# Kernel optimization log

Measured on AMD Instinct MI355X. Metric: run time of the kernel, lower is better.

## Reference

```python
import jax, jax.numpy as jnp
import numpy as np

N = 50000      # nodes
E = 800000     # edges
D_IN = 128     # embedding_dim
H = 4          # g_num_heads
D = 64         # g_hidden_dim (per head)
SLOPE = 0.2    # g_negative_slope


def setup_inputs() -> dict:
    key = jax.random.key(0)
    ks = jax.random.split(key, 16)
    def lin(k, fin, fout):
        return jax.random.normal(k, (fin, fout), jnp.float32) / np.float32(np.sqrt(fin))
    def att(k, heads):
        return jax.random.normal(k, (heads, D), jnp.float32) * np.float32(0.1)
    return {
        'x':  jax.random.normal(ks[0], (N, D_IN), jnp.float32),
        'src': jax.random.randint(ks[1], (E,), 0, N),
        'dst': jax.random.randint(ks[2], (E,), 0, N),
        'W0': lin(ks[3], D_IN, H * D), 'al0': att(ks[4], H), 'ar0': att(ks[5], H), 'b0': jnp.zeros((H * D,), jnp.float32),
        'W1': lin(ks[6], H * D, H * D), 'al1': att(ks[7], H), 'ar1': att(ks[8], H), 'b1': jnp.zeros((H * D,), jnp.float32),
        'W2': lin(ks[9], H * D, 1 * D), 'al2': att(ks[10], 1), 'ar2': att(ks[11], 1), 'b2': jnp.zeros((D,), jnp.float32),
    }


def gat_layer(x, W, al, ar, b, src, dst, heads, act):
    # x: [N, F_in] -> h: [N, heads, D]
    h = (x @ W).reshape(N, heads, D)
    el = jnp.sum(h * al, axis=-1)                      # [N, heads]
    er = jnp.sum(h * ar, axis=-1)                      # [N, heads]
    e = jax.nn.leaky_relu(el[src] + er[dst], SLOPE)    # [E, heads]
    # edge softmax over incoming edges of each dst node (numerically stable)
    m = jax.ops.segment_max(e, dst, num_segments=N)    # [N, heads]
    ee = jnp.exp(e - m[dst])
    z = jax.ops.segment_sum(ee, dst, num_segments=N)   # [N, heads]
    alpha = ee / z[dst]                                # [E, heads]
    # weighted aggregation of source features
    out = jax.ops.segment_sum(alpha[:, :, None] * h[src], dst, num_segments=N)  # [N, heads, D]
    out = out + b.reshape(1, heads, D)
    return jax.nn.elu(out) if act else out


def reference(x, src, dst, W0, al0, ar0, b0, W1, al1, ar1, b1, W2, al2, ar2, b2):
    f = gat_layer(x, W0, al0, ar0, b0, src, dst, H, True).reshape(N, H * D)
    f = gat_layer(f, W1, al1, ar1, b1, src, dst, H, True).reshape(N, H * D)
    out = gat_layer(f, W2, al2, ar2, b2, src, dst, 1, False).mean(axis=1)  # [N, D]
    return out
```

## Files before the change

kernel.cpp:

```cpp
#include <hip/hip_runtime.h>
#include <math.h>

#define NNODES 50000
#define NEDGES 800000


__global__ void k_zero_int(int* __restrict__ p, int n) {
  int i = blockIdx.x * blockDim.x + threadIdx.x;
  if (i < n) p[i] = 0;
}

__global__ void k_hist(const int* __restrict__ dst, int* __restrict__ deg) {
  int i = blockIdx.x * blockDim.x + threadIdx.x;
  if (i < NEDGES) atomicAdd(&deg[dst[i]], 1);
}

__global__ __launch_bounds__(1024) void k_scan(const int* __restrict__ deg,
                                               int* __restrict__ ptr,
                                               int* __restrict__ cur) {
  __shared__ int s_w[16];
  __shared__ int s_carry;
  const int tid = threadIdx.x;
  const int lane = tid & 63;
  const int wid = tid >> 6;
  if (tid == 0) s_carry = 0;
  __syncthreads();
  for (int base = 0; base < NNODES; base += 1024) {
    const int i = base + tid;
    const int v = (i < NNODES) ? deg[i] : 0;
    int x = v;
#pragma unroll
    for (int off = 1; off < 64; off <<= 1) {
      int t = __shfl_up(x, off);
      if (lane >= off) x += t;
    }
    if (lane == 63) s_w[wid] = x;
    __syncthreads();
    const int carry = s_carry;
    if (wid == 0) {
      int ws = (lane < 16) ? s_w[lane] : 0;
#pragma unroll
      for (int off = 1; off < 16; off <<= 1) {
        int t = __shfl_up(ws, off);
        if (lane >= off) ws += t;
      }
      if (lane < 16) s_w[lane] = ws;
    }
    __syncthreads();
    const int woff = (wid > 0) ? s_w[wid - 1] : 0;
    const int excl = carry + woff + (x - v);
    if (i < NNODES) {
      ptr[i] = excl;
      cur[i] = excl;
    }
    __syncthreads();
    if (tid == 0) s_carry = carry + s_w[15];
  }
  __syncthreads();
  if (tid == 0) ptr[NNODES] = s_carry;
}

__global__ void k_scatter(const int* __restrict__ src, const int* __restrict__ dst,
                          int* __restrict__ cur, int* __restrict__ csr) {
  int i = blockIdx.x * blockDim.x + threadIdx.x;
  if (i < NEDGES) {
    int d = dst[i];
    int p = atomicAdd(&cur[d], 1);
    csr[p] = src[i];
  }
}


template <int K, int NC, int BN>
__global__ __launch_bounds__(256) void k_gemm(const float* __restrict__ A,
                                              const float* __restrict__ B,
                                              float* __restrict__ C) {
  constexpr int BM = 128;
  constexpr int BK = 16;
  constexpr int TN = BN / 16;
  __shared__ float Ast[BK][BM + 4];
  __shared__ float Bs[BK][BN];
  const int tid = threadIdx.x;
  const int tx = tid & 15;
  const int ty = tid >> 4;
  const int rowBase = blockIdx.x * BM;
  const int colBase = blockIdx.y * BN;
  const int arow = tid >> 2;
  const int ak = (tid & 3) << 2;

  float acc[8][TN] = {};

  for (int k0 = 0; k0 < K; k0 += BK) {
#pragma unroll
    for (int rr = 0; rr < 2; ++rr) {
      const int r = arow + rr * 64;
      const int gr = rowBase + r;
      float4 av = make_float4(0.f, 0.f, 0.f, 0.f);
      if (gr < NNODES) av = *(const float4*)&A[(size_t)gr * K + k0 + ak];
      Ast[ak + 0][r] = av.x;
      Ast[ak + 1][r] = av.y;
      Ast[ak + 2][r] = av.z;
      Ast[ak + 3][r] = av.w;
    }
    if constexpr (BN == 128) {
      const int brow = tid >> 5;
      const int bcol = (tid & 31) << 2;
#pragma unroll
      for (int rr = 0; rr < 2; ++rr)
        *(float4*)&Bs[brow + rr * 8][bcol] =
            *(const float4*)&B[(size_t)(k0 + brow + rr * 8) * NC + colBase + bcol];
    } else {
      const int brow = tid >> 4;
      const int bcol = (tid & 15) << 2;
      *(float4*)&Bs[brow][bcol] =
          *(const float4*)&B[(size_t)(k0 + brow) * NC + colBase + bcol];
    }
    __syncthreads();
#pragma unroll
    for (int k = 0; k < BK; ++k) {
      float4 a0 = *(const float4*)&Ast[k][ty * 8];
      float4 a1 = *(const float4*)&Ast[k][ty * 8 + 4];
      float a[8] = {a0.x, a0.y, a0.z, a0.w, a1.x, a1.y, a1.z, a1.w};
      float b[TN];
      float4 b0 = *(const float4*)&Bs[k][tx * 4];
      b[0] = b0.x; b[1] = b0.y; b[2] = b0.z; b[3] = b0.w;
      if constexpr (TN == 8) {
        float4 b1 = *(const float4*)&Bs[k][64 + tx * 4];
        b[4] = b1.x; b[5] = b1.y; b[6] = b1.z; b[7] = b1.w;
      }
#pragma unroll
      for (int i = 0; i < 8; ++i)
#pragma unroll
        for (int j = 0; j < TN; ++j) acc[i][j] = fmaf(a[i], b[j], acc[i][j]);
    }
    __syncthreads();
  }
#pragma unroll
  for (int i = 0; i < 8; ++i) {
    const int r = rowBase + ty * 8 + i;
    if (r < NNODES) {
      {
        float4 o = make_float4(acc[i][0], acc[i][1], acc[i][2], acc[i][3]);
        *(float4*)&C[(size_t)r * NC + colBase + tx * 4] = o;
      }
      if constexpr (TN == 8) {
        float4 o = make_float4(acc[i][4], acc[i][5], acc[i][6], acc[i][7]);
        *(float4*)&C[(size_t)r * NC + colBase + 64 + tx * 4] = o;
      }
    }
  }
}


template <int HEADS>
__global__ __launch_bounds__(HEADS * 64) void k_elr(const float* __restrict__ h,
                                                    const float* __restrict__ al,
                                                    const float* __restrict__ ar,
                                                    float* __restrict__ el,
                                                    float* __restrict__ er) {
  const int n = blockIdx.x;
  const int tid = threadIdx.x;
  float hv = h[(size_t)n * HEADS * 64 + tid];
  float pl = hv * al[tid];
  float pr = hv * ar[tid];
#pragma unroll
  for (int m = 1; m < 64; m <<= 1) {
    pl += __shfl_xor(pl, m);
    pr += __shfl_xor(pr, m);
  }
  if ((tid & 63) == 0) {
    el[n * HEADS + (tid >> 6)] = pl;
    er[n * HEADS + (tid >> 6)] = pr;
  }
}


template <int HEADS, bool ACT>
__global__ __launch_bounds__(64) void k_aggregate(const float* __restrict__ h,
                                                  const float* __restrict__ el,
                                                  const float* __restrict__ er,
                                                  const int* __restrict__ ptr,
                                                  const int* __restrict__ csr,
                                                  const float* __restrict__ bias,
                                                  float* __restrict__ out) {
  constexpr int HD = HEADS * 64;
  constexpr int VEC = HEADS;
  constexpr int CH = 64 / HEADS;
  const int n = blockIdx.x;
  const int tid = threadIdx.x;
  const int head = tid / (64 / HEADS);
  const int beg = ptr[n];
  const int deg = ptr[n + 1] - beg;

  __shared__ float s_m[HEADS];
  __shared__ float s_z[HEADS];
  __shared__ int s_src[CH];
  __shared__ float s_w[64];

  {
    const int hh = tid & (HEADS - 1);
    const float ern = er[n * HEADS + hh];
    float mloc = -INFINITY;
    for (int i = tid / HEADS; i < deg; i += 64 / HEADS) {
      int s = csr[beg + i];
      float e = el[s * HEADS + hh] + ern;
      e = e > 0.f ? e : 0.2f * e;
      mloc = fmaxf(mloc, e);
    }
#pragma unroll
    for (int m = HEADS; m < 64; m <<= 1) mloc = fmaxf(mloc, __shfl_xor(mloc, m));
    float zloc = 0.f;
    for (int i = tid / HEADS; i < deg; i += 64 / HEADS) {
      int s = csr[beg + i];
      float e = el[s * HEADS + hh] + ern;
      e = e > 0.f ? e : 0.2f * e;
      zloc += expf(e - mloc);
    }
#pragma unroll
    for (int m = HEADS; m < 64; m <<= 1) zloc += __shfl_xor(zloc, m);
    if (tid < HEADS) { s_m[tid] = mloc; s_z[tid] = zloc; }
  }
  __syncthreads();
  const float invz = (deg > 0) ? 1.0f / s_z[head] : 0.f;

  float acc[VEC];
#pragma unroll
  for (int v = 0; v < VEC; ++v) acc[v] = 0.f;

  for (int c0 = 0; c0 < deg; c0 += CH) {
    const int cnt = min(CH, deg - c0);
    __syncthreads();
    {
      const int c = tid / HEADS;
      const int hh = tid & (HEADS - 1);
      if (c < cnt) {
        int s = csr[beg + c0 + c];
        if (hh == 0) s_src[c] = s;
        float e = el[s * HEADS + hh] + er[n * HEADS + hh];
        e = e > 0.f ? e : 0.2f * e;
        s_w[tid] = expf(e - s_m[hh]);
      }
    }
    __syncthreads();
    for (int c = 0; c < cnt; ++c) {
      const float w = s_w[c * HEADS + head];
      const float* hp = &h[(size_t)s_src[c] * HD + tid * VEC];
      if constexpr (VEC == 4) {
        float4 hv = *(const float4*)hp;
        acc[0] = fmaf(w, hv.x, acc[0]);
        acc[1] = fmaf(w, hv.y, acc[1]);
        acc[2] = fmaf(w, hv.z, acc[2]);
        acc[3] = fmaf(w, hv.w, acc[3]);
      } else {
        acc[0] = fmaf(w, hp[0], acc[0]);
      }
    }
  }

#pragma unroll
  for (int v = 0; v < VEC; ++v) {
    float r = acc[v] * invz + bias[tid * VEC + v];
    if (ACT) r = r > 0.f ? r : expm1f(r);
    acc[v] = r;
  }
  if constexpr (VEC == 4) {
    float4 o = make_float4(acc[0], acc[1], acc[2], acc[3]);
    *(float4*)&out[(size_t)n * HD + (tid << 2)] = o;
  } else {
    out[(size_t)n * HD + tid] = acc[0];
  }
}


extern "C" void kernel_launch(void* const* d_in, const int* in_sizes, int n_in,
                              void* d_out, int out_size, void* d_ws, size_t ws_size,
                              hipStream_t stream) {
  const float* x   = (const float*)d_in[0];
  const int*   src = (const int*)d_in[1];
  const int*   dst = (const int*)d_in[2];
  const float* W0  = (const float*)d_in[3];
  const float* al0 = (const float*)d_in[4];
  const float* ar0 = (const float*)d_in[5];
  const float* b0  = (const float*)d_in[6];
  const float* W1  = (const float*)d_in[7];
  const float* al1 = (const float*)d_in[8];
  const float* ar1 = (const float*)d_in[9];
  const float* b1  = (const float*)d_in[10];
  const float* W2  = (const float*)d_in[11];
  const float* al2 = (const float*)d_in[12];
  const float* ar2 = (const float*)d_in[13];
  const float* b2  = (const float*)d_in[14];
  float* out = (float*)d_out;

  float* hA = (float*)d_ws;
  float* fB = hA + (size_t)NNODES * 256;
  float* el = fB + (size_t)NNODES * 256;
  float* er = el + (size_t)NNODES * 4;
  int* deg  = (int*)(er + (size_t)NNODES * 4);
  int* ptr  = deg + NNODES;
  int* cur  = ptr + NNODES + 1;
  int* csr  = cur + NNODES;

  k_zero_int<<<(NNODES + 255) / 256, 256, 0, stream>>>(deg, NNODES);
  k_hist<<<(NEDGES + 255) / 256, 256, 0, stream>>>(dst, deg);
  k_scan<<<1, 1024, 0, stream>>>(deg, ptr, cur);
  k_scatter<<<(NEDGES + 255) / 256, 256, 0, stream>>>(src, dst, cur, csr);

  dim3 g128((NNODES + 127) / 128, 256 / 128);
  k_gemm<128, 256, 128><<<g128, 256, 0, stream>>>(x, W0, hA);
  k_elr<4><<<NNODES, 256, 0, stream>>>(hA, al0, ar0, el, er);
  k_aggregate<4, true><<<NNODES, 64, 0, stream>>>(hA, el, er, ptr, csr, b0, fB);
  k_gemm<256, 256, 128><<<g128, 256, 0, stream>>>(fB, W1, hA);
  k_elr<4><<<NNODES, 256, 0, stream>>>(hA, al1, ar1, el, er);
  k_aggregate<4, true><<<NNODES, 64, 0, stream>>>(hA, el, er, ptr, csr, b1, fB);
  dim3 g2((NNODES + 127) / 128, 1);
  k_gemm<256, 64, 64><<<g2, 256, 0, stream>>>(fB, W2, hA);
  k_elr<1><<<NNODES, 64, 0, stream>>>(hA, al2, ar2, el, er);
  k_aggregate<1, false><<<NNODES, 64, 0, stream>>>(hA, el, er, ptr, csr, b2, out);
}
```

Measured before the change: 753.2 us.

## Fuse attention logits into GEMM epilogue and single-pass edge softmax

Computes el/er dot products inside the GEMM epilogue with shuffle reductions, removing the separate k_elr kernels and their re-read of h. Adds register prefetch of the next A/B tile in the GEMM loop. Aggregation now computes exp(e) without subtracting the segment max and accumulates the softmax denominator alongside the weighted sum, eliminating two passes over each node's edges. This trades numerical-overflow safety for fewer passes.

```diff
diff --git a/kernel.cpp b/kernel.cpp
--- a/kernel.cpp
+++ b/kernel.cpp
@@ -71,10 +71,14 @@
 }
 
 
-template <int K, int NC, int BN>
+template <int K, int NC, int BN, int HEADS>
 __global__ __launch_bounds__(256) void k_gemm(const float* __restrict__ A,
                                               const float* __restrict__ B,
-                                              float* __restrict__ C) {
+                                              float* __restrict__ C,
+                                              const float* __restrict__ al,
+                                              const float* __restrict__ ar,
+                                              float* __restrict__ el,
+                                              float* __restrict__ er) {
   constexpr int BM = 128;
   constexpr int BK = 16;
   constexpr int TN = BN / 16;
@@ -87,40 +91,59 @@
   const int colBase = blockIdx.y * BN;
   const int arow = tid >> 2;
   const int ak = (tid & 3) << 2;
-
-  float acc[8][TN] = {};
-
-  for (int k0 = 0; k0 < K; k0 += BK) {
-#pragma unroll
-    for (int rr = 0; rr < 2; ++rr) {
-      const int r = arow + rr * 64;
-      const int gr = rowBase + r;
-      float4 av = make_float4(0.f, 0.f, 0.f, 0.f);
-      if (gr < NNODES) av = *(const float4*)&A[(size_t)gr * K + k0 + ak];
-      Ast[ak + 0][r] = av.x;
-      Ast[ak + 1][r] = av.y;
-      Ast[ak + 2][r] = av.z;
-      Ast[ak + 3][r] = av.w;
-    }
+  const bool v0 = (rowBase + arow) < NNODES;
+  const bool v1 = (rowBase + arow + 64) < NNODES;
+  const float* a0p = A + (size_t)(rowBase + arow) * K + ak;
+  const float* a1p = A + (size_t)(rowBase + arow + 64) * K + ak;
+
+  float4 avr[2];
+  float4 bvr[2];
+  const float4 z4 = make_float4(0.f, 0.f, 0.f, 0.f);
+
+  auto load_tile = [&](int k0) {
+    avr[0] = v0 ? *(const float4*)(a0p + k0) : z4;
+    avr[1] = v1 ? *(const float4*)(a1p + k0) : z4;
     if constexpr (BN == 128) {
       const int brow = tid >> 5;
       const int bcol = (tid & 31) << 2;
-#pragma unroll
-      for (int rr = 0; rr < 2; ++rr)
-        *(float4*)&Bs[brow + rr * 8][bcol] =
-            *(const float4*)&B[(size_t)(k0 + brow + rr * 8) * NC + colBase + bcol];
+      bvr[0] = *(const float4*)&B[(size_t)(k0 + brow) * NC + colBase + bcol];
+      bvr[1] = *(const float4*)&B[(size_t)(k0 + brow + 8) * NC + colBase + bcol];
     } else {
       const int brow = tid >> 4;
       const int bcol = (tid & 15) << 2;
-      *(float4*)&Bs[brow][bcol] =
-          *(const float4*)&B[(size_t)(k0 + brow) * NC + colBase + bcol];
-    }
-    __syncthreads();
+      bvr[0] = *(const float4*)&B[(size_t)(k0 + brow) * NC + colBase + bcol];
+    }
+  };
+
+  float acc[8][TN] = {};
+  load_tile(0);
+
+  for (int k0 = 0; k0 < K; k0 += BK) {
+#pragma unroll
+    for (int rr = 0; rr < 2; ++rr) {
+      const int r = arow + rr * 64;
+      Ast[ak + 0][r] = avr[rr].x;
+      Ast[ak + 1][r] = avr[rr].y;
+      Ast[ak + 2][r] = avr[rr].z;
+      Ast[ak + 3][r] = avr[rr].w;
+    }
+    if constexpr (BN == 128) {
+      const int brow = tid >> 5;
+      const int bcol = (tid & 31) << 2;
+      *(float4*)&Bs[brow][bcol] = bvr[0];
+      *(float4*)&Bs[brow + 8][bcol] = bvr[1];
+    } else {
+      const int brow = tid >> 4;
+      const int bcol = (tid & 15) << 2;
+      *(float4*)&Bs[brow][bcol] = bvr[0];
+    }
+    __syncthreads();
+    if (k0 + BK < K) load_tile(k0 + BK);
 #pragma unroll
     for (int k = 0; k < BK; ++k) {
-      float4 a0 = *(const float4*)&Ast[k][ty * 8];
-      float4 a1 = *(const float4*)&Ast[k][ty * 8 + 4];
-      float a[8] = {a0.x, a0.y, a0.z, a0.w, a1.x, a1.y, a1.z, a1.w};
+      float4 fa0 = *(const float4*)&Ast[k][ty * 8];
+      float4 fa1 = *(const float4*)&Ast[k][ty * 8 + 4];
+      float a[8] = {fa0.x, fa0.y, fa0.z, fa0.w, fa1.x, fa1.y, fa1.z, fa1.w};
       float b[TN];
       float4 b0 = *(const float4*)&Bs[k][tx * 4];
       b[0] = b0.x; b[1] = b0.y; b[2] = b0.z; b[3] = b0.w;
@@ -135,42 +158,52 @@
     }
     __syncthreads();
   }
+
+  const int head0 = colBase >> 6;
+  float4 alA = *(const float4*)&al[colBase + tx * 4];
+  float4 arA = *(const float4*)&ar[colBase + tx * 4];
+  float4 alB = z4, arB = z4;
+  if constexpr (TN == 8) {
+    alB = *(const float4*)&al[colBase + 64 + tx * 4];
+    arB = *(const float4*)&ar[colBase + 64 + tx * 4];
+  }
+
 #pragma unroll
   for (int i = 0; i < 8; ++i) {
     const int r = rowBase + ty * 8 + i;
-    if (r < NNODES) {
-      {
-        float4 o = make_float4(acc[i][0], acc[i][1], acc[i][2], acc[i][3]);
-        *(float4*)&C[(size_t)r * NC + colBase + tx * 4] = o;
-      }
+    const bool vr = r < NNODES;
+    if (vr) {
+      float4 o = make_float4(acc[i][0], acc[i][1], acc[i][2], acc[i][3]);
+      *(float4*)&C[(size_t)r * NC + colBase + tx * 4] = o;
       if constexpr (TN == 8) {
-        float4 o = make_float4(acc[i][4], acc[i][5], acc[i][6], acc[i][7]);
-        *(float4*)&C[(size_t)r * NC + colBase + 64 + tx * 4] = o;
-      }
-    }
-  }
-}
-
-
-template <int HEADS>
-__global__ __launch_bounds__(HEADS * 64) void k_elr(const float* __restrict__ h,
-                                                    const float* __restrict__ al,
-                                                    const float* __restrict__ ar,
-                                                    float* __restrict__ el,
-                                                    float* __restrict__ er) {
-  const int n = blockIdx.x;
-  const int tid = threadIdx.x;
-  float hv = h[(size_t)n * HEADS * 64 + tid];
-  float pl = hv * al[tid];
-  float pr = hv * ar[tid];
-#pragma unroll
-  for (int m = 1; m < 64; m <<= 1) {
-    pl += __shfl_xor(pl, m);
-    pr += __shfl_xor(pr, m);
-  }
-  if ((tid & 63) == 0) {
-    el[n * HEADS + (tid >> 6)] = pl;
-    er[n * HEADS + (tid >> 6)] = pr;
+        float4 o2 = make_float4(acc[i][4], acc[i][5], acc[i][6], acc[i][7]);
+        *(float4*)&C[(size_t)r * NC + colBase + 64 + tx * 4] = o2;
+      }
+    }
+    float pea = acc[i][0] * alA.x + acc[i][1] * alA.y + acc[i][2] * alA.z + acc[i][3] * alA.w;
+    float pra = acc[i][0] * arA.x + acc[i][1] * arA.y + acc[i][2] * arA.z + acc[i][3] * arA.w;
+    float peb = 0.f, prb = 0.f;
+    if constexpr (TN == 8) {
+      peb = acc[i][4] * alB.x + acc[i][5] * alB.y + acc[i][6] * alB.z + acc[i][7] * alB.w;
+      prb = acc[i][4] * arB.x + acc[i][5] * arB.y + acc[i][6] * arB.z + acc[i][7] * arB.w;
+    }
+#pragma unroll
+    for (int m = 1; m < 16; m <<= 1) {
+      pea += __shfl_xor(pea, m);
+      pra += __shfl_xor(pra, m);
+      if constexpr (TN == 8) {
+        peb += __shfl_xor(peb, m);
+        prb += __shfl_xor(prb, m);
+      }
+    }
+    if (tx == 0 && vr) {
+      el[r * HEADS + head0] = pea;
+      er[r * HEADS + head0] = pra;
+      if constexpr (TN == 8) {
+        el[r * HEADS + head0 + 1] = peb;
+        er[r * HEADS + head0 + 1] = prb;
+      }
+    }
   }
 }
 
@@ -192,54 +225,30 @@
   const int beg = ptr[n];
   const int deg = ptr[n + 1] - beg;
 
-  __shared__ float s_m[HEADS];
   __shared__ float s_z[HEADS];
   __shared__ int s_src[CH];
   __shared__ float s_w[64];
 
-  {
-    const int hh = tid & (HEADS - 1);
-    const float ern = er[n * HEADS + hh];
-    float mloc = -INFINITY;
-    for (int i = tid / HEADS; i < deg; i += 64 / HEADS) {
-      int s = csr[beg + i];
+  const int hh = tid & (HEADS - 1);
+  const int cslot = tid / HEADS;
+  const float ern = er[n * HEADS + hh];
+
+  float zacc = 0.f;
+  float acc[VEC];
+#pragma unroll
+  for (int v = 0; v < VEC; ++v) acc[v] = 0.f;
+
+  for (int c0 = 0; c0 < deg; c0 += CH) {
+    const int cnt = min(CH, deg - c0);
+    __syncthreads();
+    if (cslot < cnt) {
+      int s = csr[beg + c0 + cslot];
+      if (hh == 0) s_src[cslot] = s;
       float e = el[s * HEADS + hh] + ern;
       e = e > 0.f ? e : 0.2f * e;
-      mloc = fmaxf(mloc, e);
-    }
-#pragma unroll
-    for (int m = HEADS; m < 64; m <<= 1) mloc = fmaxf(mloc, __shfl_xor(mloc, m));
-    float zloc = 0.f;
-    for (int i = tid / HEADS; i < deg; i += 64 / HEADS) {
-      int s = csr[beg + i];
-      float e = el[s * HEADS + hh] + ern;
-      e = e > 0.f ? e : 0.2f * e;
-      zloc += expf(e - mloc);
-    }
-#pragma unroll
-    for (int m = HEADS; m < 64; m <<= 1) zloc += __shfl_xor(zloc, m);
-    if (tid < HEADS) { s_m[tid] = mloc; s_z[tid] = zloc; }
-  }
-  __syncthreads();
-  const float invz = (deg > 0) ? 1.0f / s_z[head] : 0.f;
-
-  float acc[VEC];
-#pragma unroll
-  for (int v = 0; v < VEC; ++v) acc[v] = 0.f;
-
-  for (int c0 = 0; c0 < deg; c0 += CH) {
-    const int cnt = min(CH, deg - c0);
-    __syncthreads();
-    {
-      const int c = tid / HEADS;
-      const int hh = tid & (HEADS - 1);
-      if (c < cnt) {
-        int s = csr[beg + c0 + c];
-        if (hh == 0) s_src[c] = s;
-        float e = el[s * HEADS + hh] + er[n * HEADS + hh];
-        e = e > 0.f ? e : 0.2f * e;
-        s_w[tid] = expf(e - s_m[hh]);
-      }
+      float w = expf(e);
+      s_w[tid] = w;
+      zacc += w;
     }
     __syncthreads();
     for (int c = 0; c < cnt; ++c) {
@@ -256,6 +265,12 @@
       }
     }
   }
+
+#pragma unroll
+  for (int m = HEADS; m < 64; m <<= 1) zacc += __shfl_xor(zacc, m);
+  if (tid < HEADS) s_z[tid] = zacc;
+  __syncthreads();
+  const float invz = (deg > 0) ? 1.0f / s_z[head] : 0.f;
 
 #pragma unroll
   for (int v = 0; v < VEC; ++v) {
@@ -307,14 +322,11 @@
   k_scatter<<<(NEDGES + 255) / 256, 256, 0, stream>>>(src, dst, cur, csr);
 
   dim3 g128((NNODES + 127) / 128, 256 / 128);
-  k_gemm<128, 256, 128><<<g128, 256, 0, stream>>>(x, W0, hA);
-  k_elr<4><<<NNODES, 256, 0, stream>>>(hA, al0, ar0, el, er);
+  k_gemm<128, 256, 128, 4><<<g128, 256, 0, stream>>>(x, W0, hA, al0, ar0, el, er);
   k_aggregate<4, true><<<NNODES, 64, 0, stream>>>(hA, el, er, ptr, csr, b0, fB);
-  k_gemm<256, 256, 128><<<g128, 256, 0, stream>>>(fB, W1, hA);
-  k_elr<4><<<NNODES, 256, 0, stream>>>(hA, al1, ar1, el, er);
+  k_gemm<256, 256, 128, 4><<<g128, 256, 0, stream>>>(fB, W1, hA, al1, ar1, el, er);
   k_aggregate<4, true><<<NNODES, 64, 0, stream>>>(hA, el, er, ptr, csr, b1, fB);
   dim3 g2((NNODES + 127) / 128, 1);
-  k_gemm<256, 64, 64><<<g2, 256, 0, stream>>>(fB, W2, hA);
-  k_elr<1><<<NNODES, 64, 0, stream>>>(hA, al2, ar2, el, er);
+  k_gemm<256, 64, 64, 1><<<g2, 256, 0, stream>>>(fB, W2, hA, al2, ar2, el, er);
   k_aggregate<1, false><<<NNODES, 64, 0, stream>>>(hA, el, er, ptr, csr, b2, out);
 }
```

Result: faster. 729.8 us (-3.1%).
